# Kernel tuning notes

Hardware: AMD Instinct MI355X
Metric: run time of the kernel (lower is better)

## Reference

```python
import jax, jax.numpy as jnp
import numpy as np

N_NODES = 50000
N_EDGES = 800000
IN_CH = 128
OUT_CH = 128
TIME_DIM = 64


def setup_inputs() -> dict:
    key = jax.random.key(0)
    ks = jax.random.split(key, 7)
    x = jax.random.normal(ks[0], (N_NODES, IN_CH), dtype=jnp.float32)
    edge_index = jax.random.randint(ks[1], (2, N_EDGES), 0, N_NODES, dtype=jnp.int64)
    edge_t = jax.random.uniform(ks[2], (N_EDGES,), dtype=jnp.float32)
    # parameters
    freqs = jax.random.normal(ks[3], (TIME_DIM // 2,), dtype=jnp.float32)
    fan = IN_CH + TIME_DIM
    lim = float(np.sqrt(1.0 / fan))
    lin_w = jax.random.uniform(ks[4], (OUT_CH, fan), minval=-lim, maxval=lim, dtype=jnp.float32)
    lin_b = jax.random.uniform(ks[5], (OUT_CH,), minval=-lim, maxval=lim, dtype=jnp.float32)
    glim = float(np.sqrt(6.0 / (1 + OUT_CH)))
    attn = jax.random.uniform(ks[6], (1, OUT_CH), minval=-glim, maxval=glim, dtype=jnp.float32)
    return {"x": x, "edge_index": edge_index, "edge_t": edge_t,
            "freqs": freqs, "lin_w": lin_w, "lin_b": lin_b, "attn": attn}


def reference(x, edge_index, edge_t, freqs, lin_w, lin_b, attn):
    src, dst = edge_index[0], edge_index[1]
    n_nodes = x.shape[0]
    # time encoding: [E, time_dim]
    ang = edge_t[:, None] * freqs * (2.0 * jnp.pi)
    edge_attr = jnp.concatenate([jnp.sin(ang), jnp.cos(ang)], axis=-1)
    # gather source features and project: h = tanh(Linear(cat(x_j, te)))
    msg = jnp.concatenate([x[src], edge_attr], axis=-1)        # [E, in+time]
    h = jnp.tanh(msg @ lin_w.T + lin_b)                        # [E, out]
    # segment softmax over destination nodes
    alpha = (h * attn).sum(axis=-1)                            # [E]
    seg_max = jax.ops.segment_max(alpha, dst, num_segments=n_nodes)
    ex = jnp.exp(alpha - seg_max[dst])
    denom = jax.ops.segment_sum(ex, dst, num_segments=n_nodes)
    w = ex / (denom[dst] + 1e-16)
    # scatter-add aggregation
    out = jax.ops.segment_sum(h * w[:, None], dst, num_segments=n_nodes)
    return out
```

## Files before the change

### kernel.cpp

```cpp
#include <hip/hip_runtime.h>
#include <hip/hip_bf16.h>
#include <math.h>

#define IN_CHN 128
#define OUT_CHN 128
#define KD 192
#define TM 64
#define HXP 136

typedef __bf16 bf16x8 __attribute__((ext_vector_type(8)));
typedef float f32x4 __attribute__((ext_vector_type(4)));

static __device__ __forceinline__ unsigned short f2b(float f) {
    return __builtin_bit_cast(unsigned short, (__bf16)f);
}
static __device__ __forceinline__ float b2f(unsigned short b) {
    return __uint_as_float(((unsigned int)b) << 16);
}
static __device__ __forceinline__ float fast_tanh(float x) {
    float e = __expf(2.0f * x);
    return 1.0f - 2.0f * __builtin_amdgcn_rcpf(e + 1.0f);
}

#define GLL16(gsrc, ldst) \
    __builtin_amdgcn_global_load_lds( \
        (const __attribute__((address_space(1))) unsigned int*)(gsrc), \
        (__attribute__((address_space(3))) unsigned int*)(ldst), 16, 0, 0)

#define LDS_BARRIER() do { \
    asm volatile("s_waitcnt lgkmcnt(0)" ::: "memory"); \
    __builtin_amdgcn_s_barrier(); \
    __builtin_amdgcn_sched_barrier(0); \
} while (0)


__global__ __launch_bounds__(256) void cvt_init(const float* __restrict__ x,
    unsigned short* __restrict__ xb, int* __restrict__ deg,
    int* __restrict__ side_node, long long n8, int Nn, int nb)
{
    long long i = (long long)blockIdx.x * 256 + threadIdx.x;
    if (i < n8) {
        const float4* src = (const float4*)(x + i * 8);
        float4 v0 = src[0], v1 = src[1];
        ushort4 p0 = { f2b(v0.x), f2b(v0.y), f2b(v0.z), f2b(v0.w) };
        ushort4 p1 = { f2b(v1.x), f2b(v1.y), f2b(v1.z), f2b(v1.w) };
        *(ushort4*)(xb + i * 8)     = p0;
        *(ushort4*)(xb + i * 8 + 4) = p1;
    }
    int t = (int)i;
    if (t < Nn) deg[t] = 0;
    if (t < nb) side_node[t] = -1;
}


__global__ __launch_bounds__(256) void count_deg(const int* __restrict__ ei,
                                                 int* __restrict__ deg, int E) {
    int e = blockIdx.x * 256 + threadIdx.x;
    if (e < E) atomicAdd(&deg[ei[E + e]], 1);
}

static __device__ __forceinline__ int wave_incl_scan(int v, int lane) {
    #pragma unroll
    for (int off = 1; off < 64; off <<= 1) {
        int t = __shfl_up(v, off);
        if (lane >= off) v += t;
    }
    return v;
}

__global__ __launch_bounds__(256) void scan_local(const int* __restrict__ deg,
    int* __restrict__ offs, int* __restrict__ partial, int Nn)
{
    __shared__ int wsum[4];
    int tid = threadIdx.x, lane = tid & 63, wid = tid >> 6;
    int i = blockIdx.x * 256 + tid;
    int v = (i < Nn) ? deg[i] : 0;
    int incl = wave_incl_scan(v, lane);
    if (lane == 63) wsum[wid] = incl;
    __syncthreads();
    int wpre = 0;
    for (int w = 0; w < wid; ++w) wpre += wsum[w];
    if (i < Nn) offs[i] = wpre + incl - v;
    if (tid == 255) partial[blockIdx.x] = wpre + incl;
}

__global__ __launch_bounds__(256) void finalize2(int* __restrict__ offs,
    const int* __restrict__ partial, int* __restrict__ cursor,
    int Nn, int E, int nblk)
{
    __shared__ int wsum[4];
    int b = blockIdx.x, tid = threadIdx.x, lane = tid & 63, wid = tid >> 6;
    int v = (tid < b && tid < nblk) ? partial[tid] : 0;
    #pragma unroll
    for (int off = 32; off > 0; off >>= 1) v += __shfl_xor(v, off);
    if (lane == 0) wsum[wid] = v;
    __syncthreads();
    int bp = wsum[0] + wsum[1] + wsum[2] + wsum[3];
    int i = b * 256 + tid;
    if (i < Nn) {
        int o = offs[i] + bp;
        offs[i] = o; cursor[i] = o;
        if (i == Nn - 1) offs[Nn] = E;
    }
}

__global__ __launch_bounds__(256) void fill_perm(const int* __restrict__ ei,
    const float* __restrict__ et, int* __restrict__ cursor,
    uint2* __restrict__ mt, int E)
{
    int e = blockIdx.x * 256 + threadIdx.x;
    if (e < E) {
        int d = ei[E + e];
        int pos = atomicAdd(&cursor[d], 1);
        mt[pos] = make_uint2((unsigned)ei[e], __float_as_uint(et[e]));
    }
}


__device__ __forceinline__ void load_meta(const uint2* __restrict__ mt,
    int tile, int E, int rbase, int g, int trow, int sv[2], float& tsv)
{
    int e0 = tile * TM;
    #pragma unroll
    for (int i = 0; i < 2; ++i) {
        int e = e0 + rbase + i * 4 + g;
        sv[i] = (int)mt[e < E ? e : E - 1].x;
    }
    int el = e0 + trow;
    tsv = __uint_as_float(mt[el < E ? el : E - 1].y);
}

__global__ __launch_bounds__(512) void gemm_fused(
    const unsigned short* __restrict__ xb, const uint2* __restrict__ mt,
    const int* __restrict__ offs,
    const float* __restrict__ freqs, const float* __restrict__ lw,
    const float* __restrict__ lb, const float* __restrict__ attn,
    float* __restrict__ out, float* __restrict__ den_g,
    int* __restrict__ side_node, float* __restrict__ side_den,
    float* __restrict__ side_val,
    int E, int Nn, int n_tiles, int kq, int kr)
{
    __shared__ unsigned short xs[2][TM][128];
    __shared__ unsigned short te[2][TM * 64];
    __shared__ unsigned short hx[TM * HXP];
    __shared__ float exs[2][TM];

    const int b    = blockIdx.x;
    const int t0   = b * kq + min(b, kr);
    const int cnt  = kq + (b < kr ? 1 : 0);
    if (cnt <= 0 || t0 >= n_tiles) return;
    const int tend = min(t0 + cnt, n_tiles);
    const int be0  = t0 * TM;
    const int bend = min(tend * TM, E);

    const int tid  = threadIdx.x;
    const int lane = tid & 63;
    const int wv   = tid >> 6;
    const int c16  = lane & 15;
    const int g    = lane >> 4;
    const int wbase = wv * 16;
    const int rbase = wv * 8;
    const int trow  = tid >> 3;
    const int tpart = tid & 7;
    const int sub  = lane >> 4;
    const int chl  = lane & 15;

    bf16x8 Wf[6];
    #pragma unroll
    for (int kk = 0; kk < 6; ++kk) {
        const float* wp = lw + (size_t)(wbase + c16) * KD + kk * 32 + g * 8;
        float4 v0 = *(const float4*)wp;
        float4 v1 = *(const float4*)(wp + 4);
        bf16x8 bb;
        bb[0] = (__bf16)v0.x; bb[1] = (__bf16)v0.y; bb[2] = (__bf16)v0.z; bb[3] = (__bf16)v0.w;
        bb[4] = (__bf16)v1.x; bb[5] = (__bf16)v1.y; bb[6] = (__bf16)v1.z; bb[7] = (__bf16)v1.w;
        Wf[kk] = bb;
    }
    const f32x4 bias_v = *(const f32x4*)(lb   + wbase + g * 4);
    const f32x4 attn_v = *(const f32x4*)(attn + wbase + g * 4);

    const float coff = (tpart >= 4) ? 1.5707963267948966f : 0.0f;
    float frv[8];
    #pragma unroll
    for (int j = 0; j < 8; ++j) frv[j] = freqs[(tpart & 3) * 8 + j] * 6.283185307179586f;

    int n0;
    {
        int lo = 0, hi = Nn;
        while (lo + 1 < hi) {
            int mid = (lo + hi) >> 1;
            if (offs[mid] <= be0) lo = mid; else hi = mid;
        }
        n0 = lo;
    }
    int cur_node = n0 + ((wv - (n0 & 7)) & 7);
    float a[8];
    #pragma unroll
    for (int q = 0; q < 8; ++q) a[q] = 0.0f;
    float den = 0.0f;

    float ts_nxt;
    int sv_nxt[2];
    {
        int sv0[2]; float ts0;
        load_meta(mt, t0, E, rbase, g, trow, sv0, ts0);
        #pragma unroll
        for (int i = 0; i < 2; ++i) {
            const int rlo = (rbase + i * 4 + g) & 15;
            const unsigned short* gsrc = xb + (size_t)sv0[i] * IN_CHN + ((c16 ^ rlo) * 8);
            GLL16(gsrc, &xs[0][rbase + i * 4][0]);
        }
        float v[8];
        #pragma unroll
        for (int j = 0; j < 8; ++j)
            v[j] = __sinf(ts0 * frv[j] + coff);
        unsigned short* tr = &te[0][trow * 64];
        int slot = (tpart ^ (trow & 7)) * 8;
        *(ushort4*)(tr + slot)     = (ushort4){ f2b(v[0]), f2b(v[1]), f2b(v[2]), f2b(v[3]) };
        *(ushort4*)(tr + slot + 4) = (ushort4){ f2b(v[4]), f2b(v[5]), f2b(v[6]), f2b(v[7]) };
        if (tid < TM) exs[0][tid] = 0.0f;

        int t1 = t0 + 1;
        load_meta(mt, t1 < tend ? t1 : tend - 1, E, rbase, g, trow, sv_nxt, ts_nxt);
    }

    int cur = 0;
    for (int tile = t0; tile < tend; ++tile) {
        const int e0 = tile * TM;
        const int e1 = e0 + TM;

        {
            float v[8];
            #pragma unroll
            for (int j = 0; j < 8; ++j)
                v[j] = __sinf(ts_nxt * frv[j] + coff);
            unsigned short* tr = &te[cur ^ 1][trow * 64];
            int slot = (tpart ^ (trow & 7)) * 8;
            *(ushort4*)(tr + slot)     = (ushort4){ f2b(v[0]), f2b(v[1]), f2b(v[2]), f2b(v[3]) };
            *(ushort4*)(tr + slot + 4) = (ushort4){ f2b(v[4]), f2b(v[5]), f2b(v[6]), f2b(v[7]) };
        }
        int sv2[2]; float ts2;
        {
            int t2 = tile + 2;
            load_meta(mt, t2 < tend ? t2 : tend - 1, E, rbase, g, trow, sv2, ts2);
        }

        __syncthreads();

        if (tile + 1 < tend) {
            #pragma unroll
            for (int i = 0; i < 2; ++i) {
                const int rlo = (rbase + i * 4 + g) & 15;
                const unsigned short* gsrc = xb + (size_t)sv_nxt[i] * IN_CHN + ((c16 ^ rlo) * 8);
                GLL16(gsrc, &xs[cur ^ 1][rbase + i * 4][0]);
            }
        }
        if (tid < TM) exs[cur ^ 1][tid] = 0.0f;

        f32x4 acc[4];
        #pragma unroll
        for (int mi = 0; mi < 4; ++mi) acc[mi] = (f32x4){0.f, 0.f, 0.f, 0.f};

        __builtin_amdgcn_s_setprio(1);
        const unsigned short* xsc = &xs[cur][0][0];
        const unsigned short* tec = &te[cur][0];
        #pragma unroll
        for (int mi = 0; mi < 4; ++mi) {
            const int r = mi * 16 + c16;
            const unsigned short* xrow = xsc + r * 128;
            #pragma unroll
            for (int kk = 0; kk < 4; ++kk) {
                const int slot = ((kk << 2) + g) ^ c16;
                bf16x8 av = __builtin_bit_cast(bf16x8, *(const uint4*)(xrow + slot * 8));
                acc[mi] = __builtin_amdgcn_mfma_f32_16x16x32_bf16(Wf[kk], av, acc[mi], 0, 0, 0);
            }
            const unsigned short* trw = tec + r * 64;
            bf16x8 s8 = __builtin_bit_cast(bf16x8, *(const uint4*)(trw + ((g ^ (r & 7)) * 8)));
            bf16x8 c8 = __builtin_bit_cast(bf16x8, *(const uint4*)(trw + (((g + 4) ^ (r & 7)) * 8)));
            acc[mi] = __builtin_amdgcn_mfma_f32_16x16x32_bf16(Wf[4], s8, acc[mi], 0, 0, 0);
            acc[mi] = __builtin_amdgcn_mfma_f32_16x16x32_bf16(Wf[5], c8, acc[mi], 0, 0, 0);
        }
        __builtin_amdgcn_s_setprio(0);

        #pragma unroll
        for (int mi = 0; mi < 4; ++mi) {
            const int r = mi * 16 + c16;
            f32x4 z = acc[mi];
            float p = 0.0f;
            #pragma unroll
            for (int q = 0; q < 4; ++q) {
                float h = fast_tanh(z[q] + bias_v[q]);
                z[q] = h;
                p = fmaf(h, attn_v[q], p);
            }
            ushort4 pv = (ushort4){ f2b(z[0]), f2b(z[1]), f2b(z[2]), f2b(z[3]) };
            *(ushort4*)&hx[r * HXP + wbase + g * 4] = pv;
            p += __shfl_xor(p, 16);
            p += __shfl_xor(p, 32);
            if (g == 0) atomicAdd(&exs[cur][r], p);
        }

        LDS_BARRIER();

        while (cur_node < Nn) {
            int s  = offs[cur_node];
            if (s >= e1) break;
            int en = offs[cur_node + 1];
            int lo = s > e0 ? s : e0;
            int hi = en < e1 ? en : e1;
            for (int i = lo + sub; i < hi; i += 4) {
                int li = i - e0;
                float ex = __expf(exs[cur][li]);
                uint4 hv = *(const uint4*)&hx[li * HXP + chl * 8];
                den += ex;
                unsigned int hw[4] = { hv.x, hv.y, hv.z, hv.w };
                #pragma unroll
                for (int q = 0; q < 4; ++q) {
                    a[2*q]   = fmaf(ex, b2f((unsigned short)(hw[q] & 0xFFFFu)), a[2*q]);
                    a[2*q+1] = fmaf(ex, b2f((unsigned short)(hw[q] >> 16)),     a[2*q+1]);
                }
            }
            if (en <= e1) {
                #pragma unroll
                for (int q = 0; q < 8; ++q) {
                    a[q] += __shfl_xor(a[q], 16);
                    a[q] += __shfl_xor(a[q], 32);
                }
                float ds = den + __shfl_xor(den, 16);
                ds += __shfl_xor(ds, 32);
                if (sub == 0) {
                    float* op = out + (size_t)cur_node * OUT_CHN + chl * 8;
                    *(float4*)op       = (float4){a[0], a[1], a[2], a[3]};
                    *(float4*)(op + 4) = (float4){a[4], a[5], a[6], a[7]};
                    if (chl == 0) den_g[cur_node] = ds;
                }
                #pragma unroll
                for (int q = 0; q < 8; ++q) a[q] = 0.0f;
                den = 0.0f;
                cur_node += 8;
            } else break;
        }

        ts_nxt = ts2;
        sv_nxt[0] = sv2[0]; sv_nxt[1] = sv2[1];
        cur ^= 1;
    }

    if (cur_node < Nn) {
        int s = offs[cur_node];
        if (s < bend && offs[cur_node + 1] > bend) {
            #pragma unroll
            for (int q = 0; q < 8; ++q) {
                a[q] += __shfl_xor(a[q], 16);
                a[q] += __shfl_xor(a[q], 32);
            }
            float ds = den + __shfl_xor(den, 16);
            ds += __shfl_xor(ds, 32);
            if (sub == 0) {
                float* sv = side_val + (size_t)b * OUT_CHN + chl * 8;
                *(float4*)sv       = (float4){a[0], a[1], a[2], a[3]};
                *(float4*)(sv + 4) = (float4){a[4], a[5], a[6], a[7]};
                if (chl == 0) {
                    side_den[b] = ds;
                    side_node[b] = cur_node;
                }
            }
        }
    }
}


__global__ __launch_bounds__(256) void fixup(const int* __restrict__ side_node,
    const float* __restrict__ side_den, const float* __restrict__ side_val,
    float* __restrict__ out, float* __restrict__ den_g, int nb)
{
    int w = (blockIdx.x * 256 + threadIdx.x) >> 6;
    int lane = threadIdx.x & 63;
    if (w >= nb) return;
    int node = side_node[w];
    if (node < 0) return;
    const float* sv = side_val + (size_t)w * OUT_CHN;
    float* op = out + (size_t)node * OUT_CHN;
    atomicAdd(op + lane * 2,     sv[lane * 2]);
    atomicAdd(op + lane * 2 + 1, sv[lane * 2 + 1]);
    if (lane == 0) atomicAdd(&den_g[node], side_den[w]);
}


__global__ __launch_bounds__(256) void normalize(float* __restrict__ out,
    const float* __restrict__ den_g, const int* __restrict__ offs, int Nn)
{
    int gid = blockIdx.x * 256 + threadIdx.x;
    int n = gid >> 5;
    if (n >= Nn) return;
    int c = (gid & 31) * 4;
    float4* p = (float4*)(out + (size_t)n * OUT_CHN + c);
    if (offs[n + 1] == offs[n]) { *p = (float4){0, 0, 0, 0}; return; }
    float rs = __builtin_amdgcn_rcpf(den_g[n] + 1e-16f);
    float4 v = *p;
    v.x *= rs; v.y *= rs; v.z *= rs; v.w *= rs;
    *p = v;
}


extern "C" void kernel_launch(void* const* d_in, const int* in_sizes, int n_in,
                              void* d_out, int out_size, void* d_ws, size_t ws_size,
                              hipStream_t stream) {
    const float* x     = (const float*)d_in[0];
    const int*   ei    = (const int*)d_in[1];
    const float* et    = (const float*)d_in[2];
    const float* freqs = (const float*)d_in[3];
    const float* lw    = (const float*)d_in[4];
    const float* lb    = (const float*)d_in[5];
    const float* attn  = (const float*)d_in[6];
    float* out = (float*)d_out;

    const int E  = in_sizes[2];
    const int Nn = in_sizes[0] / IN_CHN;
    const int NB = 512;

    char* ws = (char*)d_ws;
    uint2* mt      = (uint2*)ws;         size_t off = (size_t)E * sizeof(uint2);
    unsigned short* xb = (unsigned short*)(ws + off); off += (size_t)Nn * IN_CHN * sizeof(unsigned short);
    float* den_g   = (float*)(ws + off); off += (size_t)Nn * sizeof(float);
    int*   deg     = (int*)(ws + off);   off += (size_t)Nn * sizeof(int);
    int*   offs    = (int*)(ws + off);   off += (size_t)(Nn + 1) * sizeof(int);
    int*   cursor  = (int*)(ws + off);   off += (size_t)Nn * sizeof(int);
    int*   partial = (int*)(ws + off);   off += 1024 * sizeof(int);
    int*   side_node = (int*)(ws + off); off += (size_t)NB * sizeof(int);
    float* side_den  = (float*)(ws + off); off += (size_t)NB * sizeof(float);
    float* side_val  = (float*)(ws + off);

    const int nblk = (Nn + 255) / 256;
    const int eblk = (E + 255) / 256;

    long long n8 = (long long)Nn * IN_CHN / 8;
    cvt_init<<<(unsigned)((n8 + 255) / 256), 256, 0, stream>>>(x, xb, deg, side_node, n8, Nn, NB);

    count_deg<<<eblk, 256, 0, stream>>>(ei, deg, E);
    scan_local<<<nblk, 256, 0, stream>>>(deg, offs, partial, Nn);
    finalize2<<<nblk, 256, 0, stream>>>(offs, partial, cursor, Nn, E, nblk);
    fill_perm<<<eblk, 256, 0, stream>>>(ei, et, cursor, mt, E);

    const int n_tiles = (E + TM - 1) / TM;
    const int kq = n_tiles / NB, kr = n_tiles % NB;
    gemm_fused<<<NB, 512, 0, stream>>>(xb, mt, offs, freqs, lw, lb, attn,
                                       out, den_g, side_node, side_den, side_val,
                                       E, Nn, n_tiles, kq, kr);

    fixup<<<(NB * 64 + 255) / 256, 256, 0, stream>>>(side_node, side_den, side_val,
                                                     out, den_g, NB);

    normalize<<<(Nn * 32 + 255) / 256, 256, 0, stream>>>(out, den_g, offs, Nn);
}
```

Measured before the change: 234.7 us.

## Halve edge tile size and size grid from occupancy query

The edge tile shrinks from 64 to 32 rows. Each wave now gathers one x row per lane group instead of two, and time-encoding work is spread as 4 values per thread across 16 parts per row. The smaller tile cuts shared memory and registers per block, so the persistent grid is now sized as 256 times the reported resident blocks per CU (capped at 4) instead of a fixed 512. The trade-off is smaller MFMA batches per barrier, more loop iterations and more barrier overhead per edge, plus a host-side occupancy query on every launch.

```diff
diff --git a/kernel.cpp b/kernel.cpp
--- a/kernel.cpp
+++ b/kernel.cpp
@@ -5,7 +5,7 @@
 #define IN_CHN 128
 #define OUT_CHN 128
 #define KD 192
-#define TM 64
+#define TM 32
 #define HXP 136
 
 typedef __bf16 bf16x8 __attribute__((ext_vector_type(8)));
@@ -118,14 +118,11 @@
 
 
 __device__ __forceinline__ void load_meta(const uint2* __restrict__ mt,
-    int tile, int E, int rbase, int g, int trow, int sv[2], float& tsv)
+    int tile, int E, int rbase, int g, int trow, int& sv, float& tsv)
 {
     int e0 = tile * TM;
-    #pragma unroll
-    for (int i = 0; i < 2; ++i) {
-        int e = e0 + rbase + i * 4 + g;
-        sv[i] = (int)mt[e < E ? e : E - 1].x;
-    }
+    int e = e0 + rbase + g;
+    sv = (int)mt[e < E ? e : E - 1].x;
     int el = e0 + trow;
     tsv = __uint_as_float(mt[el < E ? el : E - 1].y);
 }
@@ -159,9 +156,9 @@
     const int c16  = lane & 15;
     const int g    = lane >> 4;
     const int wbase = wv * 16;
-    const int rbase = wv * 8;
-    const int trow  = tid >> 3;
-    const int tpart = tid & 7;
+    const int rbase = wv * 4;
+    const int trow  = tid >> 4;
+    const int tpart = tid & 15;
     const int sub  = lane >> 4;
     const int chl  = lane & 15;
 
@@ -179,10 +176,12 @@
     const f32x4 bias_v = *(const f32x4*)(lb   + wbase + g * 4);
     const f32x4 attn_v = *(const f32x4*)(attn + wbase + g * 4);
 
-    const float coff = (tpart >= 4) ? 1.5707963267948966f : 0.0f;
-    float frv[8];
+    const float coff = (tpart >= 8) ? 1.5707963267948966f : 0.0f;
+    float frv[4];
     #pragma unroll
-    for (int j = 0; j < 8; ++j) frv[j] = freqs[(tpart & 3) * 8 + j] * 6.283185307179586f;
+    for (int j = 0; j < 4; ++j) frv[j] = freqs[(tpart & 7) * 4 + j] * 6.283185307179586f;
+    const int tslot = (tpart & 1) * 4;
+    const int tgran = tpart >> 1;
 
     int n0;
     {
@@ -200,24 +199,22 @@
     float den = 0.0f;
 
     float ts_nxt;
-    int sv_nxt[2];
+    int sv_nxt;
     {
-        int sv0[2]; float ts0;
+        int sv0; float ts0;
         load_meta(mt, t0, E, rbase, g, trow, sv0, ts0);
+        {
+            const int rlo = (rbase + g) & 15;
+            const unsigned short* gsrc = xb + (size_t)sv0 * IN_CHN + ((c16 ^ rlo) * 8);
+            GLL16(gsrc, &xs[0][rbase][0]);
+        }
+        float v[4];
         #pragma unroll
-        for (int i = 0; i < 2; ++i) {
-            const int rlo = (rbase + i * 4 + g) & 15;
-            const unsigned short* gsrc = xb + (size_t)sv0[i] * IN_CHN + ((c16 ^ rlo) * 8);
-            GLL16(gsrc, &xs[0][rbase + i * 4][0]);
-        }
-        float v[8];
-        #pragma unroll
-        for (int j = 0; j < 8; ++j)
+        for (int j = 0; j < 4; ++j)
             v[j] = __sinf(ts0 * frv[j] + coff);
         unsigned short* tr = &te[0][trow * 64];
-        int slot = (tpart ^ (trow & 7)) * 8;
-        *(ushort4*)(tr + slot)     = (ushort4){ f2b(v[0]), f2b(v[1]), f2b(v[2]), f2b(v[3]) };
-        *(ushort4*)(tr + slot + 4) = (ushort4){ f2b(v[4]), f2b(v[5]), f2b(v[6]), f2b(v[7]) };
+        int slot = ((tgran ^ (trow & 7)) * 8) + tslot;
+        *(ushort4*)(tr + slot) = (ushort4){ f2b(v[0]), f2b(v[1]), f2b(v[2]), f2b(v[3]) };
         if (tid < TM) exs[0][tid] = 0.0f;
 
         int t1 = t0 + 1;
@@ -230,16 +227,15 @@
         const int e1 = e0 + TM;
 
         {
-            float v[8];
+            float v[4];
             #pragma unroll
-            for (int j = 0; j < 8; ++j)
+            for (int j = 0; j < 4; ++j)
                 v[j] = __sinf(ts_nxt * frv[j] + coff);
             unsigned short* tr = &te[cur ^ 1][trow * 64];
-            int slot = (tpart ^ (trow & 7)) * 8;
-            *(ushort4*)(tr + slot)     = (ushort4){ f2b(v[0]), f2b(v[1]), f2b(v[2]), f2b(v[3]) };
-            *(ushort4*)(tr + slot + 4) = (ushort4){ f2b(v[4]), f2b(v[5]), f2b(v[6]), f2b(v[7]) };
-        }
-        int sv2[2]; float ts2;
+            int slot = ((tgran ^ (trow & 7)) * 8) + tslot;
+            *(ushort4*)(tr + slot) = (ushort4){ f2b(v[0]), f2b(v[1]), f2b(v[2]), f2b(v[3]) };
+        }
+        int sv2; float ts2;
         {
             int t2 = tile + 2;
             load_meta(mt, t2 < tend ? t2 : tend - 1, E, rbase, g, trow, sv2, ts2);
@@ -248,24 +244,21 @@
         __syncthreads();
 
         if (tile + 1 < tend) {
-            #pragma unroll
-            for (int i = 0; i < 2; ++i) {
-                const int rlo = (rbase + i * 4 + g) & 15;
-                const unsigned short* gsrc = xb + (size_t)sv_nxt[i] * IN_CHN + ((c16 ^ rlo) * 8);
-                GLL16(gsrc, &xs[cur ^ 1][rbase + i * 4][0]);
-            }
+            const int rlo = (rbase + g) & 15;
+            const unsigned short* gsrc = xb + (size_t)sv_nxt * IN_CHN + ((c16 ^ rlo) * 8);
+            GLL16(gsrc, &xs[cur ^ 1][rbase][0]);
         }
         if (tid < TM) exs[cur ^ 1][tid] = 0.0f;
 
-        f32x4 acc[4];
-        #pragma unroll
-        for (int mi = 0; mi < 4; ++mi) acc[mi] = (f32x4){0.f, 0.f, 0.f, 0.f};
+        f32x4 acc[2];
+        acc[0] = (f32x4){0.f, 0.f, 0.f, 0.f};
+        acc[1] = (f32x4){0.f, 0.f, 0.f, 0.f};
 
         __builtin_amdgcn_s_setprio(1);
         const unsigned short* xsc = &xs[cur][0][0];
         const unsigned short* tec = &te[cur][0];
         #pragma unroll
-        for (int mi = 0; mi < 4; ++mi) {
+        for (int mi = 0; mi < 2; ++mi) {
             const int r = mi * 16 + c16;
             const unsigned short* xrow = xsc + r * 128;
             #pragma unroll
@@ -283,7 +276,7 @@
         __builtin_amdgcn_s_setprio(0);
 
         #pragma unroll
-        for (int mi = 0; mi < 4; ++mi) {
+        for (int mi = 0; mi < 2; ++mi) {
             const int r = mi * 16 + c16;
             f32x4 z = acc[mi];
             float p = 0.0f;
@@ -342,7 +335,7 @@
         }
 
         ts_nxt = ts2;
-        sv_nxt[0] = sv2[0]; sv_nxt[1] = sv2[1];
+        sv_nxt = sv2;
         cur ^= 1;
     }
 
@@ -417,7 +410,12 @@
 
     const int E  = in_sizes[2];
     const int Nn = in_sizes[0] / IN_CHN;
-    const int NB = 512;
+
+    int maxb = 0;
+    if (hipOccupancyMaxActiveBlocksPerMultiprocessor(&maxb, gemm_fused, 512, 0)
+            != hipSuccess || maxb < 1) maxb = 2;
+    if (maxb > 4) maxb = 4;
+    const int NB = 256 * maxb;
 
     char* ws = (char*)d_ws;
     uint2* mt      = (uint2*)ws;         size_t off = (size_t)E * sizeof(uint2);
@@ -427,8 +425,8 @@
     int*   offs    = (int*)(ws + off);   off += (size_t)(Nn + 1) * sizeof(int);
     int*   cursor  = (int*)(ws + off);   off += (size_t)Nn * sizeof(int);
     int*   partial = (int*)(ws + off);   off += 1024 * sizeof(int);
-    int*   side_node = (int*)(ws + off); off += (size_t)NB * sizeof(int);
-    float* side_den  = (float*)(ws + off); off += (size_t)NB * sizeof(float);
+    int*   side_node = (int*)(ws + off); off += 1024 * sizeof(int);
+    float* side_den  = (float*)(ws + off); off += 1024 * sizeof(float);
     float* side_val  = (float*)(ws + off);
 
     const int nblk = (Nn + 255) / 256;
```

Result: slower. 343.8 us (+46.5%).

## Fuse degree counting into conversion and normalize in-kernel, merging fixup/normalize

Applied to the files above, without the earlier changes.

Degree counting now runs inside the bf16 conversion kernel, with deg zeroed by an async memset, which removes one launch. Nodes whose edge segment lies entirely inside one block are normalized directly in the GEMM kernel epilogue. Boundary nodes are combined and normalized in a merged fixup kernel that also zero-fills empty nodes, replacing the full-output normalize pass. This drops a read-modify-write sweep over the whole output. It relies on each boundary node being split across at most two blocks, since fixup2 does a plain read-add-write instead of atomics.

```diff
diff --git a/kernel.cpp b/kernel.cpp
--- a/kernel.cpp
+++ b/kernel.cpp
@@ -34,9 +34,10 @@
 } while (0)
 
 
-__global__ __launch_bounds__(256) void cvt_init(const float* __restrict__ x,
-    unsigned short* __restrict__ xb, int* __restrict__ deg,
-    int* __restrict__ side_node, long long n8, int Nn, int nb)
+__global__ __launch_bounds__(256) void cvt_cnt(const float* __restrict__ x,
+    unsigned short* __restrict__ xb, const int* __restrict__ ei,
+    int* __restrict__ deg, int* __restrict__ side_node,
+    long long n8, int E, int nb)
 {
     long long i = (long long)blockIdx.x * 256 + threadIdx.x;
     if (i < n8) {
@@ -48,16 +49,10 @@
         *(ushort4*)(xb + i * 8 + 4) = p1;
     }
     int t = (int)i;
-    if (t < Nn) deg[t] = 0;
+    if (t < E) atomicAdd(&deg[ei[E + t]], 1);
     if (t < nb) side_node[t] = -1;
 }
 
-
-__global__ __launch_bounds__(256) void count_deg(const int* __restrict__ ei,
-                                                 int* __restrict__ deg, int E) {
-    int e = blockIdx.x * 256 + threadIdx.x;
-    if (e < E) atomicAdd(&deg[ei[E + e]], 1);
-}
 
 static __device__ __forceinline__ int wave_incl_scan(int v, int lane) {
     #pragma unroll
@@ -330,9 +325,15 @@
                 ds += __shfl_xor(ds, 32);
                 if (sub == 0) {
                     float* op = out + (size_t)cur_node * OUT_CHN + chl * 8;
-                    *(float4*)op       = (float4){a[0], a[1], a[2], a[3]};
-                    *(float4*)(op + 4) = (float4){a[4], a[5], a[6], a[7]};
-                    if (chl == 0) den_g[cur_node] = ds;
+                    if (s >= be0) {
+                        float rs = __builtin_amdgcn_rcpf(ds + 1e-16f);
+                        *(float4*)op       = (float4){a[0]*rs, a[1]*rs, a[2]*rs, a[3]*rs};
+                        *(float4*)(op + 4) = (float4){a[4]*rs, a[5]*rs, a[6]*rs, a[7]*rs};
+                    } else {
+                        *(float4*)op       = (float4){a[0], a[1], a[2], a[3]};
+                        *(float4*)(op + 4) = (float4){a[4], a[5], a[6], a[7]};
+                        if (chl == 0) den_g[cur_node] = ds;
+                    }
                 }
                 #pragma unroll
                 for (int q = 0; q < 8; ++q) a[q] = 0.0f;
@@ -370,36 +371,34 @@
 }
 
 
-__global__ __launch_bounds__(256) void fixup(const int* __restrict__ side_node,
+__global__ __launch_bounds__(256) void fixup2(const int* __restrict__ side_node,
     const float* __restrict__ side_den, const float* __restrict__ side_val,
-    float* __restrict__ out, float* __restrict__ den_g, int nb)
-{
-    int w = (blockIdx.x * 256 + threadIdx.x) >> 6;
-    int lane = threadIdx.x & 63;
-    if (w >= nb) return;
-    int node = side_node[w];
-    if (node < 0) return;
-    const float* sv = side_val + (size_t)w * OUT_CHN;
-    float* op = out + (size_t)node * OUT_CHN;
-    atomicAdd(op + lane * 2,     sv[lane * 2]);
-    atomicAdd(op + lane * 2 + 1, sv[lane * 2 + 1]);
-    if (lane == 0) atomicAdd(&den_g[node], side_den[w]);
-}
-
-
-__global__ __launch_bounds__(256) void normalize(float* __restrict__ out,
-    const float* __restrict__ den_g, const int* __restrict__ offs, int Nn)
-{
-    int gid = blockIdx.x * 256 + threadIdx.x;
-    int n = gid >> 5;
-    if (n >= Nn) return;
-    int c = (gid & 31) * 4;
-    float4* p = (float4*)(out + (size_t)n * OUT_CHN + c);
-    if (offs[n + 1] == offs[n]) { *p = (float4){0, 0, 0, 0}; return; }
-    float rs = __builtin_amdgcn_rcpf(den_g[n] + 1e-16f);
-    float4 v = *p;
-    v.x *= rs; v.y *= rs; v.z *= rs; v.w *= rs;
-    *p = v;
+    const int* __restrict__ offs,
+    float* __restrict__ out, const float* __restrict__ den_g, int nb, int Nn)
+{
+    long long gid = (long long)blockIdx.x * 256 + threadIdx.x;
+    if (gid < (long long)nb * 64) {
+        int w = (int)(gid >> 6);
+        int lane = (int)(gid & 63);
+        int node = side_node[w];
+        if (node < 0) return;
+        const float* sv = side_val + (size_t)w * OUT_CHN;
+        float* op = out + (size_t)node * OUT_CHN;
+        float rs = __builtin_amdgcn_rcpf(den_g[node] + side_den[w] + 1e-16f);
+        float2 o = *(float2*)(op + lane * 2);
+        float2 s = *(const float2*)(sv + lane * 2);
+        o.x = (o.x + s.x) * rs;
+        o.y = (o.y + s.y) * rs;
+        *(float2*)(op + lane * 2) = o;
+    } else {
+        int n = (int)(gid - (long long)nb * 64);
+        if (n >= Nn) return;
+        if (offs[n + 1] == offs[n]) {
+            float* op = out + (size_t)n * OUT_CHN;
+            for (int c = 0; c < OUT_CHN; c += 4)
+                *(float4*)(op + c) = (float4){0, 0, 0, 0};
+        }
+    }
 }
 
 
@@ -427,17 +426,20 @@
     int*   offs    = (int*)(ws + off);   off += (size_t)(Nn + 1) * sizeof(int);
     int*   cursor  = (int*)(ws + off);   off += (size_t)Nn * sizeof(int);
     int*   partial = (int*)(ws + off);   off += 1024 * sizeof(int);
-    int*   side_node = (int*)(ws + off); off += (size_t)NB * sizeof(int);
-    float* side_den  = (float*)(ws + off); off += (size_t)NB * sizeof(float);
+    int*   side_node = (int*)(ws + off); off += 1024 * sizeof(int);
+    float* side_den  = (float*)(ws + off); off += 1024 * sizeof(float);
     float* side_val  = (float*)(ws + off);
 
     const int nblk = (Nn + 255) / 256;
     const int eblk = (E + 255) / 256;
 
+    hipMemsetAsync(deg, 0, (size_t)Nn * sizeof(int), stream);
+
     long long n8 = (long long)Nn * IN_CHN / 8;
-    cvt_init<<<(unsigned)((n8 + 255) / 256), 256, 0, stream>>>(x, xb, deg, side_node, n8, Nn, NB);
-
-    count_deg<<<eblk, 256, 0, stream>>>(ei, deg, E);
+    long long cgrid = n8 > (long long)E ? n8 : (long long)E;
+    cvt_cnt<<<(unsigned)((cgrid + 255) / 256), 256, 0, stream>>>(
+        x, xb, ei, deg, side_node, n8, E, NB);
+
     scan_local<<<nblk, 256, 0, stream>>>(deg, offs, partial, Nn);
     finalize2<<<nblk, 256, 0, stream>>>(offs, partial, cursor, Nn, E, nblk);
     fill_perm<<<eblk, 256, 0, stream>>>(ei, et, cursor, mt, E);
@@ -448,8 +450,7 @@
                                        out, den_g, side_node, side_den, side_val,
                                        E, Nn, n_tiles, kq, kr);
 
-    fixup<<<(NB * 64 + 255) / 256, 256, 0, stream>>>(side_node, side_den, side_val,
-                                                     out, den_g, NB);
-
-    normalize<<<(Nn * 32 + 255) / 256, 256, 0, stream>>>(out, den_g, offs, Nn);
-}
+    long long fthreads = (long long)NB * 64 + Nn;
+    fixup2<<<(unsigned)((fthreads + 255) / 256), 256, 0, stream>>>(
+        side_node, side_den, side_val, offs, out, den_g, NB, Nn);
+}
```

After: 230.1 us. Within noise of the previous version (-2.0%).
